# Kernel tuning notes

Measured on AMD Instinct MI355X. Metric: run time of the kernel, lower is better.

Reference implementation:

```python
import jax, jax.numpy as jnp
import numpy as np

W_CHAMFER = 1.0
W_SMOOTH = 0.5
K_NEIGHBORS = 8


def _pairwise_sqdist(a, b):
    # a: [B,N,3], b: [B,M,3] -> [B,N,M] squared euclidean distances
    a2 = jnp.sum(a * a, axis=-1)  # [B,N]
    b2 = jnp.sum(b * b, axis=-1)  # [B,M]
    ab = jnp.einsum('bnd,bmd->bnm', a, b)  # [B,N,M]
    d2 = a2[:, :, None] + b2[:, None, :] - 2.0 * ab
    return jnp.maximum(d2, 0.0)


def _chamfer(pc1, pc2):
    d = jnp.sqrt(_pairwise_sqdist(pc1, pc2))  # [B,N,M] euclidean (matches torch.norm)
    d1 = jnp.min(d, axis=2)  # [B,N]
    d2 = jnp.min(d, axis=1)  # [B,M]
    return jnp.mean(d1) + jnp.mean(d2)


def _smoothness(pc, flow, k=K_NEIGHBORS):
    d2 = _pairwise_sqdist(pc, pc)  # [B,N,N]
    # k+1 nearest (squared dist preserves ordering); drop self (index 0)
    _, idx = jax.lax.top_k(-d2, k + 1)  # [B,N,k+1]
    idx = idx[:, :, 1:]  # [B,N,k]
    neighbor_flow = jax.vmap(lambda f, i: f[i])(flow, idx)  # [B,N,k,3]
    diff = flow[:, :, None, :] - neighbor_flow
    return jnp.mean(jnp.linalg.norm(diff, axis=-1))


def setup_inputs() -> dict:
    key = jax.random.key(0)
    k1, k2, k3 = jax.random.split(key, 3)
    B, N, M = 2, 8192, 8192
    pc1 = jax.random.normal(k1, (B, N, 3), dtype=jnp.float32)
    pc2 = jax.random.normal(k2, (B, M, 3), dtype=jnp.float32)
    pred_flow = jax.random.normal(k3, (B, N, 3), dtype=jnp.float32) * 0.1
    return {"pc1": pc1, "pc2": pc2, "pred_flow": pred_flow}


def reference(pc1, pc2, pred_flow):
    pc1_warped = pc1 + pred_flow
    l_chamfer = _chamfer(pc1_warped, pc2)
    l_smooth = _smoothness(pc1, pred_flow)
    return W_CHAMFER * l_chamfer + W_SMOOTH * l_smooth
```

## Files before the change

kernel.cpp:

```cpp
#include <hip/hip_runtime.h>

#define N_PTS 8192
#define BATCH 2
#define KNN 8
#define STILE 1024
#define NBLOCKS 1024

__device__ __forceinline__ void ce(unsigned &x, unsigned &y) {
    unsigned lo = min(x, y), hi = max(x, y); x = lo; y = hi;
}

__device__ __forceinline__ void insert4(unsigned o[4], unsigned key) {
    unsigned n0 = min(o[0], key);
    unsigned n1 = max(o[0], min(o[1], key));
    unsigned n2 = max(o[1], min(o[2], key));
    unsigned n3 = max(o[2], min(o[3], key));
    o[0]=n0; o[1]=n1; o[2]=n2; o[3]=n3;
}

__device__ __forceinline__ void merge_stage8(unsigned m[8], int d) {
    unsigned p[8], c[8];
    #pragma unroll
    for (int k = 0; k < 8; ++k) p[k] = (unsigned)__shfl_xor((int)m[k], d, 64);
    #pragma unroll
    for (int k = 0; k < 8; ++k) c[k] = min(m[k], p[7-k]);
    ce(c[0],c[4]); ce(c[1],c[5]); ce(c[2],c[6]); ce(c[3],c[7]);
    ce(c[0],c[2]); ce(c[1],c[3]); ce(c[4],c[6]); ce(c[5],c[7]);
    ce(c[0],c[1]); ce(c[2],c[3]); ce(c[4],c[5]); ce(c[6],c[7]);
    #pragma unroll
    for (int k = 0; k < 8; ++k) m[k] = c[k];
}

__device__ __forceinline__ void merge64(unsigned m[8]) {
    merge_stage8(m, 1); merge_stage8(m, 2); merge_stage8(m, 4);
    merge_stage8(m, 8); merge_stage8(m, 16); merge_stage8(m, 32);
}

__global__ __launch_bounds__(256, 4) void mega_kernel(
        const float* __restrict__ pc1, const float* __restrict__ pc2,
        const float* __restrict__ flow, float* __restrict__ out) {
    __shared__ float4 sq[STILE];
    __shared__ float psum[8];
    const int tid = threadIdx.x;
    const int bx = blockIdx.x;
    const int lane = tid & 63, wv = tid >> 6;

    {
        const int z  = bx >> 8;
        const int bb = z & 1, dir = z >> 1;
        const int cb = bx & 255;
        const float* P1 = pc1  + (size_t)bb * N_PTS * 3;
        const float* P2 = pc2  + (size_t)bb * N_PTS * 3;
        const float* FL = flow + (size_t)bb * N_PTS * 3;
        const int sub = tid & 15;
        const int r0 = cb * 32 + (tid >> 4) * 2;

        float mx0, my0, mz0, p20, mx1, my1, mz1, p21;
        {
            float px, py, pz;
            if (dir == 0) {
                px = P1[r0*3+0] + FL[r0*3+0];
                py = P1[r0*3+1] + FL[r0*3+1];
                pz = P1[r0*3+2] + FL[r0*3+2];
            } else {
                px = P2[r0*3+0]; py = P2[r0*3+1]; pz = P2[r0*3+2];
            }
            mx0 = -2.0f * px; my0 = -2.0f * py; mz0 = -2.0f * pz;
            p20 = fmaf(px, px, fmaf(py, py, pz * pz));
            const int r1 = r0 + 1;
            if (dir == 0) {
                px = P1[r1*3+0] + FL[r1*3+0];
                py = P1[r1*3+1] + FL[r1*3+1];
                pz = P1[r1*3+2] + FL[r1*3+2];
            } else {
                px = P2[r1*3+0]; py = P2[r1*3+1]; pz = P2[r1*3+2];
            }
            mx1 = -2.0f * px; my1 = -2.0f * py; mz1 = -2.0f * pz;
            p21 = fmaf(px, px, fmaf(py, py, pz * pz));
        }
        float b0 = __builtin_inff(), b1 = __builtin_inff();

        #pragma unroll 1
        for (int tile = 0; tile < N_PTS / STILE; ++tile) {
            const int t0 = tile * STILE;
            __syncthreads();
            #pragma unroll
            for (int u = tid; u < STILE; u += 256) {
                int g = t0 + u;
                float qx, qy, qz;
                if (dir == 0) {
                    qx = P2[g*3+0]; qy = P2[g*3+1]; qz = P2[g*3+2];
                } else {
                    qx = P1[g*3+0] + FL[g*3+0];
                    qy = P1[g*3+1] + FL[g*3+1];
                    qz = P1[g*3+2] + FL[g*3+2];
                }
                sq[u] = make_float4(qx, qy, qz, fmaf(qx, qx, fmaf(qy, qy, qz * qz)));
            }
            __syncthreads();

            #pragma unroll 8
            for (int c = 0; c < STILE / 16; ++c) {
                float4 q = sq[c * 16 + sub];
                float s0 = fmaf(mx0, q.x, fmaf(my0, q.y, fmaf(mz0, q.z, q.w)));
                float s1 = fmaf(mx1, q.x, fmaf(my1, q.y, fmaf(mz1, q.z, q.w)));
                b0 = fminf(b0, s0);
                b1 = fminf(b1, s1);
            }
        }

        #pragma unroll
        for (int d = 1; d <= 8; d <<= 1) {
            b0 = fminf(b0, __shfl_xor(b0, d, 64));
            b1 = fminf(b1, __shfl_xor(b1, d, 64));
        }
        float val = ((lane & 15) == 0)
            ? (sqrtf(fmaxf(b0 + p20, 0.0f)) + sqrtf(fmaxf(b1 + p21, 0.0f)))
            : 0.0f;
        #pragma unroll
        for (int d = 1; d < 64; d <<= 1) val += __shfl_xor(val, d, 64);
        if (lane == 0) psum[wv] = val;
    }
    __syncthreads();

    {
        const int b  = bx >> 9;
        const int sx = bx & 511;
        const int i0w = sx * 16 + wv * 4;
        const float* P = pc1  + (size_t)b * N_PTS * 3;
        const float* F = flow + (size_t)b * N_PTS * 3;

        float mx[4], my[4], mz[4], p2[4], gr[4];
        unsigned thr[4], o[4][4];
        #pragma unroll
        for (int r = 0; r < 4; ++r) {
            int i = i0w + r;
            float px = P[i*3+0], py = P[i*3+1], pz = P[i*3+2];
            mx[r] = -2.0f * px; my[r] = -2.0f * py; mz[r] = -2.0f * pz;
            p2[r] = fmaf(px, px, fmaf(py, py, pz * pz));
            gr[r] = __builtin_inff();
            thr[r] = 0xFFFFFFFFu;
            #pragma unroll
            for (int k = 0; k < 4; ++k) o[r][k] = 0xFFFFFFFFu;
        }

        auto update_thr = [&]() {
            #pragma unroll
            for (int r = 0; r < 4; ++r) {
                unsigned m0 = o[r][0], m1 = o[r][1], m2 = o[r][2], m3 = o[r][3];
                #pragma unroll
                for (int d = 1; d <= 16; d <<= 1) {
                    unsigned q0 = (unsigned)__shfl_xor((int)m0, d, 64);
                    unsigned q1 = (unsigned)__shfl_xor((int)m1, d, 64);
                    unsigned q2 = (unsigned)__shfl_xor((int)m2, d, 64);
                    unsigned q3 = (unsigned)__shfl_xor((int)m3, d, 64);
                    unsigned c0 = min(m0, q3), c1 = min(m1, q2);
                    unsigned c2 = min(m2, q1), c3 = min(m3, q0);
                    ce(c0, c2); ce(c1, c3); ce(c0, c1); ce(c2, c3);
                    m0 = c0; m1 = c1; m2 = c2; m3 = c3;
                }
                unsigned bound = max(m3, (unsigned)__shfl_xor((int)m3, 32, 64));
                thr[r] = min(thr[r], bound);
                float thr_up = __uint_as_float((thr[r] & 0xFFFFE000u) + 0x4000u);
                gr[r] = thr_up - p2[r];
            }
        };

        auto gated_span = [&](int t0, int st0, int st1) {
            #pragma unroll 2
            for (int st = st0; st < st1; ++st) {
                float4 qa = sq[st * 64 + lane];
                int j = t0 + st * 64 + lane;
                float sc[4];
                #pragma unroll
                for (int r = 0; r < 4; ++r)
                    sc[r] = fmaf(mx[r], qa.x, fmaf(my[r], qa.y, fmaf(mz[r], qa.z, qa.w)));
                #pragma unroll
                for (int r = 0; r < 4; ++r) {
                    if (__any(sc[r] <= gr[r])) {
                        float d2 = fmaxf(sc[r] + p2[r], 0.0f);
                        unsigned key = (__float_as_uint(d2) & 0xFFFFE000u) | (unsigned)j;
                        key = (j == i0w + r) ? 0xFFFFFFFFu : key;
                        insert4(o[r], key);
                    }
                }
            }
        };

        #pragma unroll 1
        for (int tile = 0; tile < N_PTS / STILE; ++tile) {
            const int t0 = tile * STILE;
            __syncthreads();
            #pragma unroll
            for (int u = tid; u < STILE; u += 256) {
                int g = t0 + u;
                float qx = P[g*3+0], qy = P[g*3+1], qz = P[g*3+2];
                sq[u] = make_float4(qx, qy, qz, fmaf(qx, qx, fmaf(qy, qy, qz * qz)));
            }
            __syncthreads();

            if (tile == 0) {
                #pragma unroll 4
                for (int st = 0; st < STILE / 64; ++st) {
                    float4 qa = sq[st * 64 + lane];
                    int j = st * 64 + lane;
                    #pragma unroll
                    for (int r = 0; r < 4; ++r) {
                        float ss = fmaf(mx[r], qa.x, fmaf(my[r], qa.y, fmaf(mz[r], qa.z, qa.w)));
                        float d2 = fmaxf(ss + p2[r], 0.0f);
                        unsigned key = (__float_as_uint(d2) & 0xFFFFE000u) | (unsigned)j;
                        key = (j == i0w + r) ? 0xFFFFFFFFu : key;
                        insert4(o[r], key);
                    }
                }
                update_thr();
            } else {
                gated_span(t0, 0, STILE / 64);
                if (tile == 1 || tile == 3) update_thr();
            }
        }

        const int sel = lane & 31;
        const int pr = sel >> 3, kk = sel & 7;
        unsigned mykey = 0xFFFFFFFFu;
        #pragma unroll
        for (int r = 0; r < 4; ++r) {
            unsigned m[8] = {o[r][0], o[r][1], o[r][2], o[r][3],
                             0xFFFFFFFFu, 0xFFFFFFFFu, 0xFFFFFFFFu, 0xFFFFFFFFu};
            merge64(m);
            if (pr == r) {
                unsigned k2 = m[0];
                #pragma unroll
                for (int t = 1; t < 8; ++t) k2 = (kk == t) ? m[t] : k2;
                mykey = k2;
            }
        }
        const int i = i0w + pr;
        const int j = (int)(mykey & (N_PTS - 1));
        float dx = F[i*3+0] - F[j*3+0];
        float dy = F[i*3+1] - F[j*3+1];
        float dz = F[i*3+2] - F[j*3+2];
        float sv = sqrtf(fmaf(dx, dx, fmaf(dy, dy, dz * dz)));
        #pragma unroll
        for (int d = 1; d < 64; d <<= 1) sv += __shfl_xor(sv, d, 64);
        if (lane == 0) psum[4 + wv] = sv;
    }
    __syncthreads();

    if (tid == 0) {
        float ch = psum[0] + psum[1] + psum[2] + psum[3];
        float sm = psum[4] + psum[5] + psum[6] + psum[7];
        atomicAdd(out, ch * (1.0f / (float)(BATCH * N_PTS))
                     + sm * (0.25f / ((float)BATCH * N_PTS * KNN)));
    }
}

extern "C" void kernel_launch(void* const* d_in, const int* in_sizes, int n_in,
                              void* d_out, int out_size, void* d_ws, size_t ws_size,
                              hipStream_t stream) {
    const float* pc1  = (const float*)d_in[0];
    const float* pc2  = (const float*)d_in[1];
    const float* flow = (const float*)d_in[2];
    float* out = (float*)d_out;

    mega_kernel<<<dim3(NBLOCKS), 256, 0, stream>>>(pc1, pc2, flow, out);
}
```

Before: 136.9 us.

## Split chamfer and smoothness work into separate blocks with higher occupancy

Each block previously did a chamfer slice and then a kNN smoothness slice back to back. Now the grid is doubled, and each block runs only one of the two phases, with its own reduction and atomic add. Launch bounds are raised to 8 waves per SIMD and the chamfer inner loop is unrolled by two with paired loads. Heterogeneous blocks can overlap and balance on the CUs, at the cost of more atomics and tighter register limits that could cause spills in the kNN path.

```diff
diff --git a/kernel.cpp b/kernel.cpp
--- a/kernel.cpp
+++ b/kernel.cpp
@@ -4,7 +4,9 @@
 #define BATCH 2
 #define KNN 8
 #define STILE 1024
-#define NBLOCKS 1024
+#define NBLK_C 1024
+#define NBLK_S 1024
+#define NBLOCKS (NBLK_C + NBLK_S)
 
 __device__ __forceinline__ void ce(unsigned &x, unsigned &y) {
     unsigned lo = min(x, y), hi = max(x, y); x = lo; y = hi;
@@ -36,16 +38,16 @@
     merge_stage8(m, 8); merge_stage8(m, 16); merge_stage8(m, 32);
 }
 
-__global__ __launch_bounds__(256, 4) void mega_kernel(
+__global__ __launch_bounds__(256, 8) void mega_kernel(
         const float* __restrict__ pc1, const float* __restrict__ pc2,
         const float* __restrict__ flow, float* __restrict__ out) {
     __shared__ float4 sq[STILE];
-    __shared__ float psum[8];
+    __shared__ float psum[4];
     const int tid = threadIdx.x;
     const int bx = blockIdx.x;
     const int lane = tid & 63, wv = tid >> 6;
 
-    {
+    if (bx < NBLK_C) {
         const int z  = bx >> 8;
         const int bb = z & 1, dir = z >> 1;
         const int cb = bx & 255;
@@ -100,12 +102,15 @@
             __syncthreads();
 
             #pragma unroll 8
-            for (int c = 0; c < STILE / 16; ++c) {
-                float4 q = sq[c * 16 + sub];
-                float s0 = fmaf(mx0, q.x, fmaf(my0, q.y, fmaf(mz0, q.z, q.w)));
-                float s1 = fmaf(mx1, q.x, fmaf(my1, q.y, fmaf(mz1, q.z, q.w)));
-                b0 = fminf(b0, s0);
-                b1 = fminf(b1, s1);
+            for (int c = 0; c < STILE / 16; c += 2) {
+                float4 qa = sq[c * 16 + sub];
+                float4 qb = sq[c * 16 + 16 + sub];
+                float s0a = fmaf(mx0, qa.x, fmaf(my0, qa.y, fmaf(mz0, qa.z, qa.w)));
+                float s1a = fmaf(mx1, qa.x, fmaf(my1, qa.y, fmaf(mz1, qa.z, qa.w)));
+                float s0b = fmaf(mx0, qb.x, fmaf(my0, qb.y, fmaf(mz0, qb.z, qb.w)));
+                float s1b = fmaf(mx1, qb.x, fmaf(my1, qb.y, fmaf(mz1, qb.z, qb.w)));
+                b0 = fminf(fminf(b0, s0a), s0b);
+                b1 = fminf(fminf(b1, s1a), s1b);
             }
         }
 
@@ -120,12 +125,16 @@
         #pragma unroll
         for (int d = 1; d < 64; d <<= 1) val += __shfl_xor(val, d, 64);
         if (lane == 0) psum[wv] = val;
-    }
-    __syncthreads();
-
-    {
-        const int b  = bx >> 9;
-        const int sx = bx & 511;
+        __syncthreads();
+
+        if (tid == 0) {
+            float ch = psum[0] + psum[1] + psum[2] + psum[3];
+            atomicAdd(out, ch * (1.0f / (float)(BATCH * N_PTS)));
+        }
+    } else {
+        const int sx9 = bx - NBLK_C;
+        const int b  = sx9 >> 9;
+        const int sx = sx9 & 511;
         const int i0w = sx * 16 + wv * 4;
         const float* P = pc1  + (size_t)b * N_PTS * 3;
         const float* F = flow + (size_t)b * N_PTS * 3;
@@ -243,15 +252,13 @@
         float sv = sqrtf(fmaf(dx, dx, fmaf(dy, dy, dz * dz)));
         #pragma unroll
         for (int d = 1; d < 64; d <<= 1) sv += __shfl_xor(sv, d, 64);
-        if (lane == 0) psum[4 + wv] = sv;
-    }
-    __syncthreads();
-
-    if (tid == 0) {
-        float ch = psum[0] + psum[1] + psum[2] + psum[3];
-        float sm = psum[4] + psum[5] + psum[6] + psum[7];
-        atomicAdd(out, ch * (1.0f / (float)(BATCH * N_PTS))
-                     + sm * (0.25f / ((float)BATCH * N_PTS * KNN)));
+        if (lane == 0) psum[wv] = sv;
+        __syncthreads();
+
+        if (tid == 0) {
+            float sm = psum[0] + psum[1] + psum[2] + psum[3];
+            atomicAdd(out, sm * (0.25f / ((float)BATCH * N_PTS * KNN)));
+        }
     }
 }
 
```

Measured after the change: 147.2 us. 1.08x slower.
